# Performance work log

Measured on AMD Instinct MI355X. Metric: run time of the kernel, lower is better.

The kernel has to match this reference:

```python
import jax, jax.numpy as jnp
import numpy as np

TOKENS, IN_F, OUT_F, GROUPS = 8192, 4096, 11008, 32  # group_size = 128


def setup_inputs() -> dict:
    key = jax.random.key(0)
    k1, k2, k3, k4, k5 = jax.random.split(key, 5)
    return {
        "quantized_x": jax.random.normal(k1, (TOKENS, IN_F), dtype=jnp.float32),
        "scales_x": jax.random.uniform(k2, (TOKENS, 1), dtype=jnp.float32),
        "weight": jax.random.normal(k3, (OUT_F, IN_F), dtype=jnp.float32),
        "weight_scales": jax.random.uniform(k4, (OUT_F, GROUPS), dtype=jnp.float32),
        "weight_offset": jax.random.normal(k5, (OUT_F, GROUPS), dtype=jnp.float32),
    }


def reference(quantized_x, scales_x, weight, weight_scales, weight_offset):
    # Dequantize activations: per-token (row) scale, no activation offset.
    x = quantized_x * scales_x  # [T, I]
    # Dequantize weights group-wise: (w - offset) * scale per group of 128.
    O, I = weight.shape
    G = weight_scales.shape[1]
    gs = I // G
    w = (weight.reshape(O, G, gs) - weight_offset[:, :, None]) * weight_scales[:, :, None]
    W = w.reshape(O, I)  # full FP weight [O, I]
    # F.linear(x, W) == x @ W.T  (bias=False)
    return jnp.einsum("ti,oi->to", x, W)
```

## Files before the change

kernel.cpp:

```cpp
#include <hip/hip_runtime.h>
#include <stdint.h>

#define M_TOK 8192
#define K_IN  4096
#define N_OUT 11008

typedef float f32x4 __attribute__((ext_vector_type(4)));
typedef __bf16 bf16x8 __attribute__((ext_vector_type(8)));

typedef const uint32_t __attribute__((address_space(1)))* gas_ptr;
typedef uint32_t __attribute__((address_space(3)))* las_ptr;

__device__ __forceinline__ uint16_t f2bf(float f) {
  uint32_t u = __float_as_uint(f);
  return (uint16_t)((u + 0x7fffu + ((u >> 16) & 1u)) >> 16);
}

__global__ __launch_bounds__(256) void dequant_x_kernel(
    const float* __restrict__ qx, const float* __restrict__ sx,
    uint16_t* __restrict__ out) {
  int idx = blockIdx.x * 256 + threadIdx.x;
  int row = idx >> 10;
  float s = sx[row];
  float4 v = reinterpret_cast<const float4*>(qx)[idx];
  ushort4 o;
  o.x = f2bf(v.x * s);
  o.y = f2bf(v.y * s);
  o.z = f2bf(v.z * s);
  o.w = f2bf(v.w * s);
  reinterpret_cast<ushort4*>(out)[idx] = o;
}

__global__ __launch_bounds__(256) void dequant_w_kernel(
    const float* __restrict__ w, const float* __restrict__ scl,
    const float* __restrict__ off, uint16_t* __restrict__ out) {
  int idx = blockIdx.x * 256 + threadIdx.x;
  int rg = idx >> 5;
  float s = scl[rg];
  float o = off[rg];
  float4 v = reinterpret_cast<const float4*>(w)[idx];
  ushort4 u;
  u.x = f2bf((v.x - o) * s);
  u.y = f2bf((v.y - o) * s);
  u.z = f2bf((v.z - o) * s);
  u.w = f2bf((v.w - o) * s);
  reinterpret_cast<ushort4*>(out)[idx] = u;
}

__global__ __launch_bounds__(512, 2) void gemm_bt_kernel(
    const uint16_t* __restrict__ A,
    const uint16_t* __restrict__ B,
    float* __restrict__ C) {
  constexpr int K = K_IN;
  constexpr int N = N_OUT;

  __shared__ __align__(128) uint16_t smem[65536];
  uint16_t* sA = smem;
  uint16_t* sB = smem + 32768;

  const int tid  = threadIdx.x;
  const int lane = tid & 63;
  const int wave = tid >> 6;
  const int wm = wave >> 2;
  const int wn = wave & 3;

  const int bid = blockIdx.x;
  const int xcd = bid & 7;
  const int wic = bid >> 3;
  const int blockM = ((xcd << 2) | (wic & 3)) << 8;
  const int blockN = (wic >> 2) << 8;

  f32x4 acc[8][4];
#pragma unroll
  for (int i = 0; i < 8; ++i)
#pragma unroll
    for (int j = 0; j < 4; ++j) acc[i][j] = {0.f, 0.f, 0.f, 0.f};

  const int dr = lane >> 3;
  const int cg = (lane & 7) ^ dr;
  const int xw = wave * 8 + dr;
  const uint16_t* aSrcBase = A + (size_t)(blockM + xw) * K + cg * 8;
  const uint16_t* bSrcBase =
      B + (size_t)(blockN + ((xw >> 5) << 6) + (xw & 31)) * K + cg * 8;

#define STAGE_A(TT, D, MQ)                                                      \
  do {                                                                          \
    _Pragma("unroll") for (int h_ = 0; h_ < 2; ++h_) {                          \
      __builtin_amdgcn_global_load_lds(                                         \
          (gas_ptr)(const void*)(aSrcBase +                                     \
                                 (size_t)(h_ * 128 + (MQ) * 64) * K +           \
                                 (size_t)(TT) * 64),                            \
          (las_ptr)(void*)(sA + (D) * 16384 +                                   \
                           (h_ * 128 + (MQ) * 64 + wave * 8) * 64),             \
          16, 0, 0);                                                            \
    }                                                                           \
  } while (0)

#define STAGE_B(TT, D, NQ)                                                      \
  do {                                                                          \
    _Pragma("unroll") for (int h_ = 0; h_ < 2; ++h_) {                          \
      __builtin_amdgcn_global_load_lds(                                         \
          (gas_ptr)(const void*)(bSrcBase +                                     \
                                 (size_t)(h_ * 128 + (NQ) * 32) * K +           \
                                 (size_t)(TT) * 64),                            \
          (las_ptr)(void*)(sB + (D) * 16384 +                                   \
                           ((NQ) * 128 + h_ * 64 + wave * 8) * 64),             \
          16, 0, 0);                                                            \
    }                                                                           \
  } while (0)

  bf16x8 af[4][2];
  bf16x8 bfr[2][2];

#define READ_A(D, MQ)                                                           \
  do {                                                                          \
    _Pragma("unroll") for (int mi_ = 0; mi_ < 4; ++mi_) {                       \
      const uint16_t* pa_ =                                                     \
          sA + (D) * 16384 +                                                    \
          (wm * 128 + (MQ) * 64 + mi_ * 16 + (lane & 15)) * 64;                 \
      _Pragma("unroll") for (int ks_ = 0; ks_ < 2; ++ks_) {                     \
        const int kc_ = ks_ * 4 + (lane >> 4);                                  \
        af[mi_][ks_] = *reinterpret_cast<const bf16x8*>(                        \
            pa_ + ((kc_ ^ (lane & 7)) << 3));                                   \
      }                                                                         \
    }                                                                           \
  } while (0)

#define READ_B(D, NQ)                                                           \
  do {                                                                          \
    _Pragma("unroll") for (int ni_ = 0; ni_ < 2; ++ni_) {                       \
      const uint16_t* pb_ =                                                     \
          sB + (D) * 16384 +                                                    \
          ((NQ) * 128 + (wn >> 1) * 64 + (wn & 1) * 32 + ni_ * 16 +             \
           (lane & 15)) * 64;                                                   \
      _Pragma("unroll") for (int ks_ = 0; ks_ < 2; ++ks_) {                     \
        const int kc_ = ks_ * 4 + (lane >> 4);                                  \
        bfr[ni_][ks_] = *reinterpret_cast<const bf16x8*>(                       \
            pb_ + ((kc_ ^ (lane & 7)) << 3));                                   \
      }                                                                         \
    }                                                                           \
  } while (0)

#define DO_MFMA(MQ, NQ)                                                         \
  do {                                                                          \
    __builtin_amdgcn_s_setprio(1);                                              \
    _Pragma("unroll") for (int ks_ = 0; ks_ < 2; ++ks_)                         \
    _Pragma("unroll") for (int mi_ = 0; mi_ < 4; ++mi_)                         \
    _Pragma("unroll") for (int ni_ = 0; ni_ < 2; ++ni_)                         \
        acc[(MQ) * 4 + mi_][(NQ) * 2 + ni_] =                                   \
            __builtin_amdgcn_mfma_f32_16x16x32_bf16(                            \
                af[mi_][ks_], bfr[ni_][ks_],                                    \
                acc[(MQ) * 4 + mi_][(NQ) * 2 + ni_], 0, 0, 0);                  \
    __builtin_amdgcn_s_setprio(0);                                              \
  } while (0)

#define BAR    __builtin_amdgcn_s_barrier()
#define LGKM0  asm volatile("s_waitcnt lgkmcnt(0)" ::: "memory")
#define VMCNT6 asm volatile("s_waitcnt vmcnt(6)" ::: "memory")

  STAGE_A(0, 0, 0);
  STAGE_B(0, 0, 0);
  STAGE_A(0, 0, 1);
  STAGE_B(0, 0, 1);
  STAGE_A(1, 1, 0);
  STAGE_B(1, 1, 1);
  STAGE_A(1, 1, 1);
  VMCNT6;
  BAR;

  for (int i = 0; i < 32; ++i) {
    const int t1 = 2 * i + 1;
    const int t2 = (2 * i + 2) & 63;
    const int t3 = (2 * i + 3) & 63;

    READ_A(0, 0);
    READ_B(0, 0);
    STAGE_B(t1, 1, 0);
    BAR; LGKM0; DO_MFMA(0, 0); BAR;

    READ_B(0, 1);
    STAGE_A(t2, 0, 0);
    BAR; LGKM0; DO_MFMA(0, 1); BAR;

    READ_A(0, 1);
    STAGE_B(t2, 0, 1);
    BAR; LGKM0; DO_MFMA(1, 1); BAR;

    READ_B(0, 0);
    STAGE_A(t2, 0, 1);
    VMCNT6;
    BAR; LGKM0; DO_MFMA(1, 0); BAR;

    READ_A(1, 0);
    READ_B(1, 0);
    STAGE_B(t2, 0, 0);
    BAR; LGKM0; DO_MFMA(0, 0); BAR;

    READ_B(1, 1);
    STAGE_A(t3, 1, 0);
    BAR; LGKM0; DO_MFMA(0, 1); BAR;

    READ_A(1, 1);
    STAGE_B(t3, 1, 1);
    BAR; LGKM0; DO_MFMA(1, 1); BAR;

    READ_B(1, 0);
    STAGE_A(t3, 1, 1);
    VMCNT6;
    BAR; LGKM0; DO_MFMA(1, 0); BAR;
  }

  const int crow0 = blockM + wm * 128 + (lane >> 4) * 4;
  const int ccol0 = blockN + wn * 64 + (lane & 15);
#pragma unroll
  for (int MI = 0; MI < 8; ++MI)
#pragma unroll
    for (int NI = 0; NI < 4; ++NI)
#pragma unroll
      for (int v = 0; v < 4; ++v)
        C[(size_t)(crow0 + MI * 16 + v) * N + (ccol0 + NI * 16)] =
            acc[MI][NI][v];

#undef STAGE_A
#undef STAGE_B
#undef READ_A
#undef READ_B
#undef DO_MFMA
#undef BAR
#undef LGKM0
#undef VMCNT6
}

extern "C" void kernel_launch(void* const* d_in, const int* in_sizes, int n_in,
                              void* d_out, int out_size, void* d_ws, size_t ws_size,
                              hipStream_t stream) {
  const float* qx   = (const float*)d_in[0];
  const float* sx   = (const float*)d_in[1];
  const float* w    = (const float*)d_in[2];
  const float* wscl = (const float*)d_in[3];
  const float* woff = (const float*)d_in[4];
  float* out = (float*)d_out;

  uint16_t* Abf = (uint16_t*)d_ws;
  uint16_t* Bbf = Abf + (size_t)M_TOK * K_IN;

  {
    int n4 = M_TOK * K_IN / 4;
    dequant_x_kernel<<<n4 / 256, 256, 0, stream>>>(qx, sx, Abf);
  }
  {
    int n4 = (int)((size_t)N_OUT * K_IN / 4);
    dequant_w_kernel<<<n4 / 256, 256, 0, stream>>>(w, wscl, woff, Bbf);
  }
  {
    dim3 grid(1376);
    gemm_bt_kernel<<<grid, 512, 0, stream>>>(Abf, Bbf, out);
  }
}
```

Measured before the change: 1.138 ms.

## Remap waves to a 4x2 grid with 64x128 warp tiles and regroup staging

Changes the wave layout inside the 256x256 block from 2x4 (128x64 per wave) to 4x2 (64x128 per wave). The A fragment is now read once per K sub-tile and reused across four N quarters, where before A was re-read for each M half. The global-to-LDS staging schedule is reorganised into a TILE macro that interleaves per-64-row A and B chunks, with vmcnt raised to 7. This aims to cut LDS reads of A per MFMA phase and rebalance the loads, but it changes the pipeline timing and how the waits cover the outstanding loads.

```diff
diff --git a/kernel.cpp b/kernel.cpp
--- a/kernel.cpp
+++ b/kernel.cpp
@@ -61,8 +61,8 @@
   const int tid  = threadIdx.x;
   const int lane = tid & 63;
   const int wave = tid >> 6;
-  const int wm = wave >> 2;
-  const int wn = wave & 3;
+  const int wm = wave >> 1;
+  const int wn = wave & 1;
 
   const int bid = blockIdx.x;
   const int xcd = bid & 7;
@@ -70,54 +70,39 @@
   const int blockM = ((xcd << 2) | (wic & 3)) << 8;
   const int blockN = (wic >> 2) << 8;
 
-  f32x4 acc[8][4];
-#pragma unroll
-  for (int i = 0; i < 8; ++i)
-#pragma unroll
-    for (int j = 0; j < 4; ++j) acc[i][j] = {0.f, 0.f, 0.f, 0.f};
+  f32x4 acc[4][8];
+#pragma unroll
+  for (int i = 0; i < 4; ++i)
+#pragma unroll
+    for (int j = 0; j < 8; ++j) acc[i][j] = {0.f, 0.f, 0.f, 0.f};
 
   const int dr = lane >> 3;
   const int cg = (lane & 7) ^ dr;
   const int xw = wave * 8 + dr;
   const uint16_t* aSrcBase = A + (size_t)(blockM + xw) * K + cg * 8;
   const uint16_t* bSrcBase =
-      B + (size_t)(blockN + ((xw >> 5) << 6) + (xw & 31)) * K + cg * 8;
-
-#define STAGE_A(TT, D, MQ)                                                      \
-  do {                                                                          \
-    _Pragma("unroll") for (int h_ = 0; h_ < 2; ++h_) {                          \
-      __builtin_amdgcn_global_load_lds(                                         \
-          (gas_ptr)(const void*)(aSrcBase +                                     \
-                                 (size_t)(h_ * 128 + (MQ) * 64) * K +           \
-                                 (size_t)(TT) * 64),                            \
-          (las_ptr)(void*)(sA + (D) * 16384 +                                   \
-                           (h_ * 128 + (MQ) * 64 + wave * 8) * 64),             \
-          16, 0, 0);                                                            \
-    }                                                                           \
-  } while (0)
-
-#define STAGE_B(TT, D, NQ)                                                      \
-  do {                                                                          \
-    _Pragma("unroll") for (int h_ = 0; h_ < 2; ++h_) {                          \
-      __builtin_amdgcn_global_load_lds(                                         \
-          (gas_ptr)(const void*)(bSrcBase +                                     \
-                                 (size_t)(h_ * 128 + (NQ) * 32) * K +           \
-                                 (size_t)(TT) * 64),                            \
-          (las_ptr)(void*)(sB + (D) * 16384 +                                   \
-                           ((NQ) * 128 + h_ * 64 + wave * 8) * 64),             \
-          16, 0, 0);                                                            \
-    }                                                                           \
-  } while (0)
+      B + (size_t)(blockN + (xw >> 5) * 128 + (xw & 31)) * K + cg * 8;
+
+#define STAGE_A1(TT, D, U)                                                      \
+  __builtin_amdgcn_global_load_lds(                                             \
+      (gas_ptr)(const void*)(aSrcBase + (size_t)((U) * 64) * K +                \
+                             (size_t)(TT) * 64),                                \
+      (las_ptr)(void*)(sA + (D) * 16384 + ((U) * 64 + wave * 8) * 64), 16, 0, 0)
+
+#define STAGE_B1(TT, D, NQ)                                                     \
+  __builtin_amdgcn_global_load_lds(                                             \
+      (gas_ptr)(const void*)(bSrcBase + (size_t)((NQ) * 32) * K +               \
+                             (size_t)(TT) * 64),                                \
+      (las_ptr)(void*)(sB + (D) * 16384 + ((NQ) * 64 + wave * 8) * 64), 16, 0, 0)
 
   bf16x8 af[4][2];
   bf16x8 bfr[2][2];
 
-#define READ_A(D, MQ)                                                           \
+#define READ_A(D)                                                               \
   do {                                                                          \
     _Pragma("unroll") for (int mi_ = 0; mi_ < 4; ++mi_) {                       \
       const uint16_t* pa_ =                                                     \
-          sA + (D) * 16384 +                                                    \
-          (wm * 128 + (MQ) * 64 + mi_ * 16 + (lane & 15)) * 64;                 \
+          sA + (D) * 16384 + (wm * 64 + mi_ * 16 + (lane & 15)) * 64;           \
       _Pragma("unroll") for (int ks_ = 0; ks_ < 2; ++ks_) {                     \
         const int kc_ = ks_ * 4 + (lane >> 4);                                  \
         af[mi_][ks_] = *reinterpret_cast<const bf16x8*>(                        \
@@ -131,8 +116,7 @@
     _Pragma("unroll") for (int ni_ = 0; ni_ < 2; ++ni_) {                       \
       const uint16_t* pb_ =                                                     \
           sB + (D) * 16384 +                                                    \
-          ((NQ) * 128 + (wn >> 1) * 64 + (wn & 1) * 32 + ni_ * 16 +             \
-           (lane & 15)) * 64;                                                   \
+          ((NQ) * 64 + wn * 32 + ni_ * 16 + (lane & 15)) * 64;                  \
       _Pragma("unroll") for (int ks_ = 0; ks_ < 2; ++ks_) {                     \
         const int kc_ = ks_ * 4 + (lane >> 4);                                  \
         bfr[ni_][ks_] = *reinterpret_cast<const bf16x8*>(                       \
@@ -141,94 +125,87 @@
     }                                                                           \
   } while (0)
 
-#define DO_MFMA(MQ, NQ)                                                         \
+#define DO_MFMA(NQ)                                                             \
   do {                                                                          \
     __builtin_amdgcn_s_setprio(1);                                              \
     _Pragma("unroll") for (int ks_ = 0; ks_ < 2; ++ks_)                         \
     _Pragma("unroll") for (int mi_ = 0; mi_ < 4; ++mi_)                         \
     _Pragma("unroll") for (int ni_ = 0; ni_ < 2; ++ni_)                         \
-        acc[(MQ) * 4 + mi_][(NQ) * 2 + ni_] =                                   \
+        acc[mi_][(NQ) * 2 + ni_] =                                              \
             __builtin_amdgcn_mfma_f32_16x16x32_bf16(                            \
-                af[mi_][ks_], bfr[ni_][ks_],                                    \
-                acc[(MQ) * 4 + mi_][(NQ) * 2 + ni_], 0, 0, 0);                  \
+                af[mi_][ks_], bfr[ni_][ks_], acc[mi_][(NQ) * 2 + ni_], 0, 0, 0);\
     __builtin_amdgcn_s_setprio(0);                                              \
   } while (0)
 
 #define BAR    __builtin_amdgcn_s_barrier()
 #define LGKM0  asm volatile("s_waitcnt lgkmcnt(0)" ::: "memory")
-#define VMCNT6 asm volatile("s_waitcnt vmcnt(6)" ::: "memory")
-
-  STAGE_A(0, 0, 0);
-  STAGE_B(0, 0, 0);
-  STAGE_A(0, 0, 1);
-  STAGE_B(0, 0, 1);
-  STAGE_A(1, 1, 0);
-  STAGE_B(1, 1, 1);
-  STAGE_A(1, 1, 1);
-  VMCNT6;
+#define VMCNT7 asm volatile("s_waitcnt vmcnt(7)" ::: "memory")
+
+#define TILE(D, D1, TN, TNN)                                                    \
+  do {                                                                          \
+           \
+    READ_A(D);                                                                  \
+    READ_B(D, 0);                                                               \
+    STAGE_B1(TN, D1, 3);                                                        \
+    BAR; LGKM0; DO_MFMA(0); BAR;                                                \
+                   \
+    READ_B(D, 1);                                                               \
+    STAGE_A1(TNN, D, 0);                                                        \
+    STAGE_A1(TNN, D, 1);                                                        \
+    STAGE_B1(TNN, D, 0);                                                        \
+    BAR; LGKM0; DO_MFMA(1); BAR;                                                \
+                          \
+    READ_B(D, 2);                                                               \
+    STAGE_A1(TNN, D, 2);                                                        \
+    STAGE_B1(TNN, D, 1);                                                        \
+    BAR; LGKM0; DO_MFMA(2); BAR;                                                \
+       \
+    READ_B(D, 3);                                                               \
+    STAGE_A1(TNN, D, 3);                                                        \
+    STAGE_B1(TNN, D, 2);                                                        \
+    VMCNT7;                                                                     \
+    BAR; LGKM0; DO_MFMA(3); BAR;                                                \
+  } while (0)
+
+#pragma unroll
+  for (int u = 0; u < 4; ++u) STAGE_A1(0, 0, u);
+#pragma unroll
+  for (int q = 0; q < 4; ++q) STAGE_B1(0, 0, q);
+#pragma unroll
+  for (int u = 0; u < 4; ++u) STAGE_A1(1, 1, u);
+#pragma unroll
+  for (int q = 0; q < 3; ++q) STAGE_B1(1, 1, q);
+  VMCNT7;
   BAR;
 
   for (int i = 0; i < 32; ++i) {
     const int t1 = 2 * i + 1;
     const int t2 = (2 * i + 2) & 63;
     const int t3 = (2 * i + 3) & 63;
-
-    READ_A(0, 0);
-    READ_B(0, 0);
-    STAGE_B(t1, 1, 0);
-    BAR; LGKM0; DO_MFMA(0, 0); BAR;
-
-    READ_B(0, 1);
-    STAGE_A(t2, 0, 0);
-    BAR; LGKM0; DO_MFMA(0, 1); BAR;
-
-    READ_A(0, 1);
-    STAGE_B(t2, 0, 1);
-    BAR; LGKM0; DO_MFMA(1, 1); BAR;
-
-    READ_B(0, 0);
-    STAGE_A(t2, 0, 1);
-    VMCNT6;
-    BAR; LGKM0; DO_MFMA(1, 0); BAR;
-
-    READ_A(1, 0);
-    READ_B(1, 0);
-    STAGE_B(t2, 0, 0);
-    BAR; LGKM0; DO_MFMA(0, 0); BAR;
-
-    READ_B(1, 1);
-    STAGE_A(t3, 1, 0);
-    BAR; LGKM0; DO_MFMA(0, 1); BAR;
-
-    READ_A(1, 1);
-    STAGE_B(t3, 1, 1);
-    BAR; LGKM0; DO_MFMA(1, 1); BAR;
-
-    READ_B(1, 0);
-    STAGE_A(t3, 1, 1);
-    VMCNT6;
-    BAR; LGKM0; DO_MFMA(1, 0); BAR;
-  }
-
-  const int crow0 = blockM + wm * 128 + (lane >> 4) * 4;
-  const int ccol0 = blockN + wn * 64 + (lane & 15);
-#pragma unroll
-  for (int MI = 0; MI < 8; ++MI)
-#pragma unroll
-    for (int NI = 0; NI < 4; ++NI)
+    TILE(0, 1, t1, t2);
+    TILE(1, 0, t2, t3);
+  }
+
+  const int crow0 = blockM + wm * 64 + (lane >> 4) * 4;
+  const int ccol0 = blockN + wn * 128 + (lane & 15);
+#pragma unroll
+  for (int MI = 0; MI < 4; ++MI)
+#pragma unroll
+    for (int NI = 0; NI < 8; ++NI)
 #pragma unroll
       for (int v = 0; v < 4; ++v)
         C[(size_t)(crow0 + MI * 16 + v) * N + (ccol0 + NI * 16)] =
             acc[MI][NI][v];
 
-#undef STAGE_A
-#undef STAGE_B
+#undef STAGE_A1
+#undef STAGE_B1
 #undef READ_A
 #undef READ_B
 #undef DO_MFMA
+#undef TILE
 #undef BAR
 #undef LGKM0
-#undef VMCNT6
+#undef VMCNT7
 }
 
 extern "C" void kernel_launch(void* const* d_in, const int* in_sizes, int n_in,
```

Result: no change. 1.151 ms (+1.2%).
